# Optimization experiments

Hardware: AMD Instinct MI355X
Metric: run time of the kernel (lower is better)

## Reference

```python
import jax, jax.numpy as jnp
import numpy as np

H = 16
D_MODEL = 1024
D_K = D_MODEL // H
WINDOW = 50
ROPE_BASE = 10000.0


def _rope_tables(seq_len, dim, dtype):
    inv_freq = 1.0 / (ROPE_BASE ** (jnp.arange(0, dim, 2, dtype=jnp.float32) / dim))
    t = jnp.arange(seq_len, dtype=jnp.float32)
    freqs = t[:, None] * inv_freq[None, :]          # [S, dim/2]
    emb = jnp.concatenate([freqs, freqs], axis=-1)  # [S, dim]
    return jnp.cos(emb).astype(dtype), jnp.sin(emb).astype(dtype)


def _rotate_half(x):
    d = x.shape[-1] // 2
    return jnp.concatenate([-x[..., d:], x[..., :d]], axis=-1)


def setup_inputs() -> dict:
    key = jax.random.key(0)
    ks = jax.random.split(key, 11)
    B, S = 2, 2048
    scale = 1.0 / np.sqrt(D_MODEL)
    inp = {
        'query': jax.random.normal(ks[0], (B, S, D_MODEL), jnp.float32),
        'key':   jax.random.normal(ks[1], (B, S, D_MODEL), jnp.float32),
        'value': jax.random.normal(ks[2], (B, S, D_MODEL), jnp.float32),
        'Wq': jax.random.normal(ks[3], (D_MODEL, D_MODEL), jnp.float32) * scale,
        'bq': jnp.zeros((D_MODEL,), jnp.float32),
        'Wk': jax.random.normal(ks[4], (D_MODEL, D_MODEL), jnp.float32) * scale,
        'bk': jnp.zeros((D_MODEL,), jnp.float32),
        'Wv': jax.random.normal(ks[5], (D_MODEL, D_MODEL), jnp.float32) * scale,
        'bv': jnp.zeros((D_MODEL,), jnp.float32),
        'Wo': jax.random.normal(ks[6], (D_MODEL, D_MODEL), jnp.float32) * scale,
        'bo': jnp.zeros((D_MODEL,), jnp.float32),
    }
    return inp


def reference(query, key, value, Wq, bq, Wk, bk, Wv, bv, Wo, bo):
    B, S, _ = query.shape
    # QKV projections (torch Linear: x @ W.T + b), split into heads -> [B,H,S,Dk]
    def proj(x, W, b):
        return (x @ W.T + b).reshape(B, S, H, D_K).transpose(0, 2, 1, 3)
    q = proj(query, Wq, bq)
    k = proj(key, Wk, bk)
    v = proj(value, Wv, bv)

    cos, sin = _rope_tables(S, D_K, q.dtype)  # [S, Dk]
    q = q * cos + _rotate_half(q) * sin
    k = k * cos + _rotate_half(k) * sin

    scores = jnp.einsum('bhqd,bhkd->bhqk', q, k) / np.sqrt(D_K)
    # sliding-window mask: |i-j| <= WINDOW
    idx = jnp.arange(S)
    dist = jnp.abs(idx[None, :] - idx[:, None])  # [S, S]
    scores = jnp.where(dist <= WINDOW, scores, jnp.asarray(-1e9, scores.dtype))

    p = jax.nn.softmax(scores, axis=-1)
    out = jnp.einsum('bhqk,bhkd->bhqd', p, v)          # [B,H,S,Dk]
    out = out.transpose(0, 2, 1, 3).reshape(B, S, D_MODEL)
    return out @ Wo.T + bo
```

## Files before the change

kernel.cpp:

```cpp
#include <hip/hip_runtime.h>
#include <hip/hip_bf16.h>
#include <math.h>

typedef __bf16 bf16_t;
typedef __bf16 bf16x8 __attribute__((ext_vector_type(8)));
typedef float floatx4 __attribute__((ext_vector_type(4)));
typedef unsigned int u32;

#define NHEAD 16

__device__ __forceinline__ void gload_lds16(const void* g, void* l) {
    __builtin_amdgcn_global_load_lds((const __attribute__((address_space(1))) u32*)g,
                                     (__attribute__((address_space(3))) u32*)l, 16, 0, 0);
}

__global__ __launch_bounds__(256) void k_prep(
    const float* __restrict__ q, const float* __restrict__ k, const float* __restrict__ v,
    const float* __restrict__ wq, const float* __restrict__ wk,
    const float* __restrict__ wv, const float* __restrict__ wo,
    bf16_t* __restrict__ Xq, bf16_t* __restrict__ Xk, bf16_t* __restrict__ Xv,
    bf16_t* __restrict__ Wqb, bf16_t* __restrict__ Wkb, bf16_t* __restrict__ Wvb,
    bf16_t* __restrict__ Wob, float* __restrict__ ct, float* __restrict__ st)
{
    int b = blockIdx.x;
    if (b < 8192) {
        const float* src; bf16_t* dst; int off;
        if      (b < 2048) { src = q;  dst = Xq;  off = b; }
        else if (b < 4096) { src = k;  dst = Xk;  off = b - 2048; }
        else if (b < 6144) { src = v;  dst = Xv;  off = b - 4096; }
        else if (b < 6656) { src = wq; dst = Wqb; off = b - 6144; }
        else if (b < 7168) { src = wk; dst = Wkb; off = b - 6656; }
        else if (b < 7680) { src = wv; dst = Wvb; off = b - 7168; }
        else               { src = wo; dst = Wob; off = b - 7680; }
        int i = (off * 256 + threadIdx.x) * 8;
        float4 a = *(const float4*)(src + i);
        float4 c = *(const float4*)(src + i + 4);
        bf16x8 o;
        o[0]=(bf16_t)a.x; o[1]=(bf16_t)a.y; o[2]=(bf16_t)a.z; o[3]=(bf16_t)a.w;
        o[4]=(bf16_t)c.x; o[5]=(bf16_t)c.y; o[6]=(bf16_t)c.z; o[7]=(bf16_t)c.w;
        *(bf16x8*)(dst + i) = o;
    } else {
        int idx = (b - 8192) * 256 + threadIdx.x;
        int s = idx >> 5, i = idx & 31;
        float e = (float)(2 * i) / 64.0f;
        float invf = 1.0f / powf(10000.0f, e);
        float ang = (float)s * invf;
        ct[idx] = cosf(ang);
        st[idx] = sinf(ang);
    }
}


__global__ __launch_bounds__(256,3) void k_gemm_qkv(
    const bf16_t* __restrict__ Xq, const bf16_t* __restrict__ Xk, const bf16_t* __restrict__ Xv,
    const bf16_t* __restrict__ Wqb, const bf16_t* __restrict__ Wkb, const bf16_t* __restrict__ Wvb,
    const float* __restrict__ bq, const float* __restrict__ bk, const float* __restrict__ bv,
    bf16_t* __restrict__ Qr, bf16_t* __restrict__ Kr, bf16_t* __restrict__ Vh,
    const float* __restrict__ ct, const float* __restrict__ st)
{
    __shared__ __align__(16) bf16_t As[2][4096];
    __shared__ __align__(16) bf16_t Bs[2][4096];

    int b0 = blockIdx.x;
    int wg = (b0 & 7) * 96 + (b0 >> 3);
    int id  = wg >> 8;
    int bid = wg & 255;

    const bf16_t* A   = (id==0) ? Xq  : (id==1) ? Xk  : Xv;
    const bf16_t* Wt  = (id==0) ? Wqb : (id==1) ? Wkb : Wvb;
    const float*  bias= (id==0) ? bq  : (id==1) ? bk  : bv;
    bf16_t* out = (id==0) ? Qr : (id==1) ? Kr : Vh;
    bool do_rope = (id < 2);

    int bm = (bid >> 3) << 7;
    int bn = (bid & 7) << 7;
    int tid = threadIdx.x;
    int l = tid & 63, wid = tid >> 6;
    int wr = wid >> 1, wc = wid & 1;
    int fr = l & 15, kg = l >> 4;

    floatx4 acc[4][4];
    #pragma unroll
    for (int i = 0; i < 4; ++i)
        #pragma unroll
        for (int j = 0; j < 4; ++j) acc[i][j] = (floatx4){0.f,0.f,0.f,0.f};

    int srow = tid >> 2;
    int scol = ((tid & 3) ^ (srow & 3)) << 3;
    const bf16_t* Ap0 = A  + ((size_t)(bm + srow) << 10) + scol;
    const bf16_t* Ap1 = A  + ((size_t)(bm + 64 + srow) << 10) + scol;
    const bf16_t* Bp0 = Wt + ((size_t)(bn + srow) << 10) + scol;
    const bf16_t* Bp1 = Wt + ((size_t)(bn + 64 + srow) << 10) + scol;

    gload_lds16(Ap0, &As[0][tid << 3]);
    gload_lds16(Ap1, &As[0][(tid + 256) << 3]);
    gload_lds16(Bp0, &Bs[0][tid << 3]);
    gload_lds16(Bp1, &Bs[0][(tid + 256) << 3]);
    __syncthreads();

    int a_off = fr * 64 + ((kg ^ (fr & 3)) << 4);
    int cur = 0;
    for (int t = 0; t < 32; ++t) {
        if (t < 31) {
            int k0 = (t + 1) << 5;
            gload_lds16(Ap0 + k0, &As[cur ^ 1][tid << 3]);
            gload_lds16(Ap1 + k0, &As[cur ^ 1][(tid + 256) << 3]);
            gload_lds16(Bp0 + k0, &Bs[cur ^ 1][tid << 3]);
            gload_lds16(Bp1 + k0, &Bs[cur ^ 1][(tid + 256) << 3]);
        }
        bf16x8 af[4], bfr[4];
        #pragma unroll
        for (int i = 0; i < 4; ++i)
            af[i]  = *(const bf16x8*)((const char*)As[cur] + (((wr << 2) + i) << 10) + a_off);
        #pragma unroll
        for (int j = 0; j < 4; ++j)
            bfr[j] = *(const bf16x8*)((const char*)Bs[cur] + (((wc << 2) + j) << 10) + a_off);
        #pragma unroll
        for (int i = 0; i < 4; ++i)
            #pragma unroll
            for (int j = 0; j < 4; ++j)
                acc[i][j] = __builtin_amdgcn_mfma_f32_16x16x32_bf16(af[i], bfr[j], acc[i][j], 0, 0, 0);
        __syncthreads();
        cur ^= 1;
    }

    int h = (bn + (wc<<6)) >> 6;
    #pragma unroll
    for (int i = 0; i < 4; ++i) {
        #pragma unroll
        for (int r = 0; r < 4; ++r) {
            int m  = bm + (wr<<6) + (i<<4) + (kg<<2) + r;
            int b_ = m >> 11, s_ = m & 2047;
            size_t ob = ((((size_t)(b_*NHEAD + h)) << 11) + s_) << 6;
            if (do_rope) {
                #pragma unroll
                for (int j = 0; j < 2; ++j) {
                    int d = (j<<4) + fr;
                    float lo = acc[i][j][r]   + bias[bn + (wc<<6) + d];
                    float hv = acc[i][j+2][r] + bias[bn + (wc<<6) + d + 32];
                    float c = ct[(s_<<5) + d], sn = st[(s_<<5) + d];
                    out[ob + d]      = (bf16_t)(lo*c - hv*sn);
                    out[ob + d + 32] = (bf16_t)(hv*c + lo*sn);
                }
            } else {
                #pragma unroll
                for (int j = 0; j < 4; ++j) {
                    int d = (j<<4) + fr;
                    out[ob + d] = (bf16_t)(acc[i][j][r] + bias[bn + (wc<<6) + d]);
                }
            }
        }
    }
}

__global__ __launch_bounds__(256,4) void k_gemm_o(
    const bf16_t* __restrict__ A, const bf16_t* __restrict__ Wt,
    const float* __restrict__ bias, float* __restrict__ out)
{
    __shared__ __align__(16) bf16_t As[2][2048];
    __shared__ __align__(16) bf16_t Bs[2][2048];

    int b0 = blockIdx.x;
    int wg = (b0 & 7) * 128 + (b0 >> 3);
    int bm = (wg >> 4) << 6;
    int bn = (wg & 15) << 6;
    int tid = threadIdx.x;
    int l = tid & 63, wid = tid >> 6;
    int fr = l & 15, kg = l >> 4;

    floatx4 acc[4];
    #pragma unroll
    for (int j = 0; j < 4; ++j) acc[j] = (floatx4){0.f,0.f,0.f,0.f};

    int srow = tid >> 2;
    int scol = ((tid & 3) ^ (srow & 3)) << 3;
    const bf16_t* Ap = A  + ((size_t)(bm + srow) << 10) + scol;
    const bf16_t* Bp = Wt + ((size_t)(bn + srow) << 10) + scol;

    gload_lds16(Ap, &As[0][tid << 3]);
    gload_lds16(Bp, &Bs[0][tid << 3]);
    __syncthreads();

    int a_off = fr * 64 + ((kg ^ (fr & 3)) << 4);
    int cur = 0;
    for (int t = 0; t < 32; ++t) {
        if (t < 31) {
            int k0 = (t + 1) << 5;
            gload_lds16(Ap + k0, &As[cur ^ 1][tid << 3]);
            gload_lds16(Bp + k0, &Bs[cur ^ 1][tid << 3]);
        }
        bf16x8 af, bfr[4];
        af = *(const bf16x8*)((const char*)As[cur] + (wid << 10) + a_off);
        #pragma unroll
        for (int j = 0; j < 4; ++j)
            bfr[j] = *(const bf16x8*)((const char*)Bs[cur] + (j << 10) + a_off);
        #pragma unroll
        for (int j = 0; j < 4; ++j)
            acc[j] = __builtin_amdgcn_mfma_f32_16x16x32_bf16(af, bfr[j], acc[j], 0, 0, 0);
        __syncthreads();
        cur ^= 1;
    }

    #pragma unroll
    for (int r = 0; r < 4; ++r) {
        int m = bm + (wid << 4) + (kg << 2) + r;
        #pragma unroll
        for (int j = 0; j < 4; ++j) {
            int n = bn + (j << 4) + fr;
            out[((size_t)m << 10) + n] = acc[j][r] + bias[n];
        }
    }
}

__global__ __launch_bounds__(256,3) void k_attn(
    const bf16_t* __restrict__ Qr, const bf16_t* __restrict__ Kr,
    const bf16_t* __restrict__ Vh, bf16_t* __restrict__ AO)
{
    __shared__ char smem[51200];
    char* KsPs = smem;
    char* VtB  = smem + 25600;

    int q0 = blockIdx.x << 6;
    int h = blockIdx.y, b_ = blockIdx.z;
    int kstart = q0 - 64; if (kstart < 0) kstart = 0;
    int kend   = q0 + 128; if (kend > 2048) kend = 2048;
    int NR = kend - kstart;

    int tid = threadIdx.x, l = tid & 63, w = tid >> 6;
    int lane16 = l & 15, hi8 = (l >> 4) << 3;

    const bf16_t* Kbase = Kr + (((((size_t)(b_*NHEAD + h)) << 11) + kstart) << 6);
    const bf16_t* Vbase = Vh + (((((size_t)(b_*NHEAD + h)) << 11) + kstart) << 6);

    #pragma unroll
    for (int it = 0; it < 6; ++it) {
        int c = tid + (it << 8);
        int y = c << 4;
        int row = y >> 7, oz = y & 127;
        int srw = row < NR ? row : NR - 1;
        int src = (srw << 7) + (oz ^ ((row & 7) << 4));
        gload_lds16((const char*)Kbase + src, KsPs + y);
    }
    #pragma unroll
    for (int it = 0; it < 6; ++it) {
        int c = tid + (it << 8);
        int jd = c >> 3, d0 = (c & 7) << 3;
        int js = jd < NR ? jd : NR - 1;
        bf16x8 v8 = *(const bf16x8*)(Vbase + (js << 6) + d0);
        #pragma unroll
        for (int t = 0; t < 8; ++t) {
            int d = d0 + t;
            int byte = d * 400 + (((jd << 1)) ^ (((d >> 3) & 7) << 4));
            *(bf16_t*)(VtB + byte) = v8[t];
        }
    }
    int qs = q0 + (w << 4) + lane16;
    const bf16_t* Qbase = Qr + (((((size_t)(b_*NHEAD + h)) << 11) + qs) << 6);
    bf16x8 qf0 = *(const bf16x8*)(Qbase + hi8);
    bf16x8 qf1 = *(const bf16x8*)(Qbase + 32 + hi8);

    __syncthreads();

    floatx4 sc[12];
    #pragma unroll
    for (int kt = 0; kt < 12; ++kt) {
        int row = (kt << 4) + lane16;
        int base = (row << 7) + (hi8 << 1);
        int swz = (row & 7) << 4;
        bf16x8 kf0 = *(const bf16x8*)(KsPs + (base ^ swz));
        bf16x8 kf1 = *(const bf16x8*)(KsPs + ((base + 64) ^ swz));
        floatx4 a = (floatx4){0.f,0.f,0.f,0.f};
        a = __builtin_amdgcn_mfma_f32_16x16x32_bf16(qf0, kf0, a, 0, 0, 0);
        a = __builtin_amdgcn_mfma_f32_16x16x32_bf16(qf1, kf1, a, 0, 0, 0);
        sc[kt] = a;
    }

    float inv_[4];
    #pragma unroll
    for (int r = 0; r < 4; ++r) {
        int qrow = q0 + (w << 4) + ((l >> 4) << 2) + r;
        float mx = -1e30f;
        #pragma unroll
        for (int kt = 0; kt < 12; ++kt) {
            int ks = kstart + (kt << 4) + lane16;
            int dd = qrow - ks; dd = dd < 0 ? -dd : dd;
            float sv = sc[kt][r] * 0.125f;
            sv = (dd <= 50 && ks < kend) ? sv : -1e30f;
            sc[kt][r] = sv;
            mx = fmaxf(mx, sv);
        }
        #pragma unroll
        for (int off = 1; off < 16; off <<= 1) mx = fmaxf(mx, __shfl_xor(mx, off));
        float sum = 0.f;
        #pragma unroll
        for (int kt = 0; kt < 12; ++kt) {
            float p = __expf(sc[kt][r] - mx);
            sc[kt][r] = p;
            sum += p;
        }
        #pragma unroll
        for (int off = 1; off < 16; off <<= 1) sum += __shfl_xor(sum, off);
        inv_[r] = 1.0f / sum;
    }

    __syncthreads();

    char* PwB = KsPs + w * 6400;
    #pragma unroll
    for (int r = 0; r < 4; ++r) {
        int prow = ((l >> 4) << 2) + r;
        int pm = ((prow >> 2) & 3) << 4;
        #pragma unroll
        for (int kt = 0; kt < 12; ++kt) {
            int keyoff = ((kt << 4) + lane16) << 1;
            *(bf16_t*)(PwB + prow * 400 + (keyoff ^ pm)) = (bf16_t)(sc[kt][r] * inv_[r]);
        }
    }

    floatx4 oc[4];
    #pragma unroll
    for (int dt = 0; dt < 4; ++dt) oc[dt] = (floatx4){0.f,0.f,0.f,0.f};
    int pm_r = ((lane16 >> 2) & 3) << 4;
    #pragma unroll
    for (int ks = 0; ks < 6; ++ks) {
        int keyoff = ((ks << 5) + hi8) << 1;
        bf16x8 pf = *(const bf16x8*)(PwB + lane16 * 400 + (keyoff ^ pm_r));
        #pragma unroll
        for (int dt = 0; dt < 4; ++dt) {
            int d = (dt << 4) + lane16;
            bf16x8 vf = *(const bf16x8*)(VtB + d * 400 + (keyoff ^ (((d >> 3) & 7) << 4)));
            oc[dt] = __builtin_amdgcn_mfma_f32_16x16x32_bf16(pf, vf, oc[dt], 0, 0, 0);
        }
    }
    #pragma unroll
    for (int dt = 0; dt < 4; ++dt)
        #pragma unroll
        for (int r = 0; r < 4; ++r) {
            int qq = q0 + (w << 4) + ((l >> 4) << 2) + r;
            AO[(((size_t)(b_ * 2048 + qq)) << 10) + (h << 6) + (dt << 4) + lane16] = (bf16_t)oc[dt][r];
        }
}

extern "C" void kernel_launch(void* const* d_in, const int* in_sizes, int n_in,
                              void* d_out, int out_size, void* d_ws, size_t ws_size,
                              hipStream_t stream)
{
    const float* query = (const float*)d_in[0];
    const float* key_  = (const float*)d_in[1];
    const float* value = (const float*)d_in[2];
    const float* Wq = (const float*)d_in[3];
    const float* bq = (const float*)d_in[4];
    const float* Wk = (const float*)d_in[5];
    const float* bk = (const float*)d_in[6];
    const float* Wv = (const float*)d_in[7];
    const float* bv = (const float*)d_in[8];
    const float* Wo = (const float*)d_in[9];
    const float* bo = (const float*)d_in[10];

    char* ws = (char*)d_ws;
    bf16_t* Xq  = (bf16_t*)(ws);
    bf16_t* Xk  = (bf16_t*)(ws + 8388608);
    bf16_t* Xv  = (bf16_t*)(ws + 16777216);
    bf16_t* Wqb = (bf16_t*)(ws + 25165824);
    bf16_t* Wkb = (bf16_t*)(ws + 27262976);
    bf16_t* Wvb = (bf16_t*)(ws + 29360128);
    bf16_t* Wob = (bf16_t*)(ws + 31457280);
    bf16_t* Qr  = (bf16_t*)(ws + 33554432);
    bf16_t* Kr  = (bf16_t*)(ws + 41943040);
    bf16_t* Vh  = (bf16_t*)(ws + 50331648);
    bf16_t* AO  = (bf16_t*)(ws + 58720256);
    float*  ct  = (float*)(ws + 67108864);
    float*  st  = (float*)(ws + 67371008);

    k_prep<<<8448, 256, 0, stream>>>(query, key_, value, Wq, Wk, Wv, Wo,
                                     Xq, Xk, Xv, Wqb, Wkb, Wvb, Wob, ct, st);
    k_gemm_qkv<<<768, 256, 0, stream>>>(Xq, Xk, Xv, Wqb, Wkb, Wvb,
                                        bq, bk, bv, Qr, Kr, Vh, ct, st);
    k_attn<<<dim3(32, 16, 2), 256, 0, stream>>>(Qr, Kr, Vh, AO);
    k_gemm_o<<<1024, 256, 0, stream>>>(AO, Wob, bo, (float*)d_out);
}
```

Baseline: 94.11 us.

## Fuse fp32-to-bf16 activation conversion into QKV GEMM loads

The QKV GEMM now stages the fp32 activations directly into LDS with an XOR swizzle and converts them to bf16 while building MFMA fragments. The separate prep pass that wrote bf16 copies of query/key/value is removed. This cuts a full read and write of the activations through global memory, at the cost of doubling LDS use for the A tile and adding conversion work inside the GEMM loop. Separately, the V-transpose staging in attention now packs two rows into one 32-bit LDS store instead of issuing scalar 16-bit stores.

```diff
diff --git a/kernel.cpp b/kernel.cpp
--- a/kernel.cpp
+++ b/kernel.cpp
@@ -6,6 +6,7 @@
 typedef __bf16 bf16x8 __attribute__((ext_vector_type(8)));
 typedef float floatx4 __attribute__((ext_vector_type(4)));
 typedef unsigned int u32;
+typedef unsigned short u16;
 
 #define NHEAD 16
 
@@ -14,33 +15,32 @@
                                      (__attribute__((address_space(3))) u32*)l, 16, 0, 0);
 }
 
+__device__ __forceinline__ bf16x8 cvt8(float4 a, float4 b) {
+    bf16x8 o;
+    o[0]=(bf16_t)a.x; o[1]=(bf16_t)a.y; o[2]=(bf16_t)a.z; o[3]=(bf16_t)a.w;
+    o[4]=(bf16_t)b.x; o[5]=(bf16_t)b.y; o[6]=(bf16_t)b.z; o[7]=(bf16_t)b.w;
+    return o;
+}
+
 __global__ __launch_bounds__(256) void k_prep(
-    const float* __restrict__ q, const float* __restrict__ k, const float* __restrict__ v,
     const float* __restrict__ wq, const float* __restrict__ wk,
     const float* __restrict__ wv, const float* __restrict__ wo,
-    bf16_t* __restrict__ Xq, bf16_t* __restrict__ Xk, bf16_t* __restrict__ Xv,
     bf16_t* __restrict__ Wqb, bf16_t* __restrict__ Wkb, bf16_t* __restrict__ Wvb,
     bf16_t* __restrict__ Wob, float* __restrict__ ct, float* __restrict__ st)
 {
     int b = blockIdx.x;
-    if (b < 8192) {
+    if (b < 2048) {
         const float* src; bf16_t* dst; int off;
-        if      (b < 2048) { src = q;  dst = Xq;  off = b; }
-        else if (b < 4096) { src = k;  dst = Xk;  off = b - 2048; }
-        else if (b < 6144) { src = v;  dst = Xv;  off = b - 4096; }
-        else if (b < 6656) { src = wq; dst = Wqb; off = b - 6144; }
-        else if (b < 7168) { src = wk; dst = Wkb; off = b - 6656; }
-        else if (b < 7680) { src = wv; dst = Wvb; off = b - 7168; }
-        else               { src = wo; dst = Wob; off = b - 7680; }
+        if      (b < 512)  { src = wq; dst = Wqb; off = b; }
+        else if (b < 1024) { src = wk; dst = Wkb; off = b - 512; }
+        else if (b < 1536) { src = wv; dst = Wvb; off = b - 1024; }
+        else               { src = wo; dst = Wob; off = b - 1536; }
         int i = (off * 256 + threadIdx.x) * 8;
         float4 a = *(const float4*)(src + i);
         float4 c = *(const float4*)(src + i + 4);
-        bf16x8 o;
-        o[0]=(bf16_t)a.x; o[1]=(bf16_t)a.y; o[2]=(bf16_t)a.z; o[3]=(bf16_t)a.w;
-        o[4]=(bf16_t)c.x; o[5]=(bf16_t)c.y; o[6]=(bf16_t)c.z; o[7]=(bf16_t)c.w;
-        *(bf16x8*)(dst + i) = o;
+        *(bf16x8*)(dst + i) = cvt8(a, c);
     } else {
-        int idx = (b - 8192) * 256 + threadIdx.x;
+        int idx = (b - 2048) * 256 + threadIdx.x;
         int s = idx >> 5, i = idx & 31;
         float e = (float)(2 * i) / 64.0f;
         float invf = 1.0f / powf(10000.0f, e);
@@ -50,15 +50,14 @@
     }
 }
 
-
 __global__ __launch_bounds__(256,3) void k_gemm_qkv(
-    const bf16_t* __restrict__ Xq, const bf16_t* __restrict__ Xk, const bf16_t* __restrict__ Xv,
+    const float* __restrict__ Xq, const float* __restrict__ Xk, const float* __restrict__ Xv,
     const bf16_t* __restrict__ Wqb, const bf16_t* __restrict__ Wkb, const bf16_t* __restrict__ Wvb,
     const float* __restrict__ bq, const float* __restrict__ bk, const float* __restrict__ bv,
     bf16_t* __restrict__ Qr, bf16_t* __restrict__ Kr, bf16_t* __restrict__ Vh,
     const float* __restrict__ ct, const float* __restrict__ st)
 {
-    __shared__ __align__(16) bf16_t As[2][4096];
+    __shared__ __align__(16) float  As[2][4096];
     __shared__ __align__(16) bf16_t Bs[2][4096];
 
     int b0 = blockIdx.x;
@@ -66,7 +65,7 @@
     int id  = wg >> 8;
     int bid = wg & 255;
 
-    const bf16_t* A   = (id==0) ? Xq  : (id==1) ? Xk  : Xv;
+    const float*  A   = (id==0) ? Xq  : (id==1) ? Xk  : Xv;
     const bf16_t* Wt  = (id==0) ? Wqb : (id==1) ? Wkb : Wvb;
     const float*  bias= (id==0) ? bq  : (id==1) ? bk  : bv;
     bf16_t* out = (id==0) ? Qr : (id==1) ? Kr : Vh;
@@ -85,36 +84,49 @@
         #pragma unroll
         for (int j = 0; j < 4; ++j) acc[i][j] = (floatx4){0.f,0.f,0.f,0.f};
 
-    int srow = tid >> 2;
-    int scol = ((tid & 3) ^ (srow & 3)) << 3;
-    const bf16_t* Ap0 = A  + ((size_t)(bm + srow) << 10) + scol;
-    const bf16_t* Ap1 = A  + ((size_t)(bm + 64 + srow) << 10) + scol;
-    const bf16_t* Bp0 = Wt + ((size_t)(bn + srow) << 10) + scol;
-    const bf16_t* Bp1 = Wt + ((size_t)(bn + 64 + srow) << 10) + scol;
-
-    gload_lds16(Ap0, &As[0][tid << 3]);
-    gload_lds16(Ap1, &As[0][(tid + 256) << 3]);
+    const char* ApB[4];
+    #pragma unroll
+    for (int it = 0; it < 4; ++it) {
+        int c = tid + (it << 8);
+        int row = c >> 3;
+        int zp = ((c & 7) << 4) ^ ((row & 7) << 4);
+        ApB[it] = (const char*)A + ((size_t)(bm + row) << 12) + zp;
+    }
+    int srowB = tid >> 2, scolB = (tid & 3) << 3;
+    const bf16_t* Bp0 = Wt + ((size_t)(bn + srowB) << 10) + scolB;
+    const bf16_t* Bp1 = Wt + ((size_t)(bn + 64 + srowB) << 10) + scolB;
+
+    #pragma unroll
+    for (int it = 0; it < 4; ++it)
+        gload_lds16(ApB[it], (char*)As[0] + ((tid + (it << 8)) << 4));
     gload_lds16(Bp0, &Bs[0][tid << 3]);
     gload_lds16(Bp1, &Bs[0][(tid + 256) << 3]);
     __syncthreads();
 
-    int a_off = fr * 64 + ((kg ^ (fr & 3)) << 4);
+    int swA = (fr & 7) << 4;
     int cur = 0;
     for (int t = 0; t < 32; ++t) {
         if (t < 31) {
-            int k0 = (t + 1) << 5;
-            gload_lds16(Ap0 + k0, &As[cur ^ 1][tid << 3]);
-            gload_lds16(Ap1 + k0, &As[cur ^ 1][(tid + 256) << 3]);
-            gload_lds16(Bp0 + k0, &Bs[cur ^ 1][tid << 3]);
-            gload_lds16(Bp1 + k0, &Bs[cur ^ 1][(tid + 256) << 3]);
-        }
+            int kA = (t + 1) << 7;
+            int kB = (t + 1) << 5;
+            #pragma unroll
+            for (int it = 0; it < 4; ++it)
+                gload_lds16(ApB[it] + kA, (char*)As[cur ^ 1] + ((tid + (it << 8)) << 4));
+            gload_lds16(Bp0 + kB, &Bs[cur ^ 1][tid << 3]);
+            gload_lds16(Bp1 + kB, &Bs[cur ^ 1][(tid + 256) << 3]);
+        }
+        const char* Ac = (const char*)As[cur];
         bf16x8 af[4], bfr[4];
         #pragma unroll
-        for (int i = 0; i < 4; ++i)
-            af[i]  = *(const bf16x8*)((const char*)As[cur] + (((wr << 2) + i) << 10) + a_off);
+        for (int i = 0; i < 4; ++i) {
+            int rowbyte = ((wr << 6) + (i << 4) + fr) << 7;
+            float4 lo = *(const float4*)(Ac + rowbyte + ((kg << 5) ^ swA));
+            float4 hi = *(const float4*)(Ac + rowbyte + (((kg << 5) + 16) ^ swA));
+            af[i] = cvt8(lo, hi);
+        }
         #pragma unroll
         for (int j = 0; j < 4; ++j)
-            bfr[j] = *(const bf16x8*)((const char*)Bs[cur] + (((wc << 2) + j) << 10) + a_off);
+            bfr[j] = *(const bf16x8*)&Bs[cur][((wc << 6) + (j << 4) + fr) * 32 + (kg << 3)];
         #pragma unroll
         for (int i = 0; i < 4; ++i)
             #pragma unroll
@@ -244,14 +256,20 @@
     #pragma unroll
     for (int it = 0; it < 6; ++it) {
         int c = tid + (it << 8);
-        int jd = c >> 3, d0 = (c & 7) << 3;
-        int js = jd < NR ? jd : NR - 1;
-        bf16x8 v8 = *(const bf16x8*)(Vbase + (js << 6) + d0);
-        #pragma unroll
-        for (int t = 0; t < 8; ++t) {
-            int d = d0 + t;
-            int byte = d * 400 + (((jd << 1)) ^ (((d >> 3) & 7) << 4));
-            *(bf16_t*)(VtB + byte) = v8[t];
+        int jd2 = c >> 4;
+        int dq  = (c & 15) << 2;
+        int j0 = jd2 << 1, j1 = j0 + 1;
+        int j0c = j0 < NR ? j0 : NR - 1;
+        int j1c = j1 < NR ? j1 : NR - 1;
+        ushort4 v0 = *(const ushort4*)(Vbase + (j0c << 6) + dq);
+        ushort4 v1 = *(const ushort4*)(Vbase + (j1c << 6) + dq);
+        u16 a0[4] = {(u16)v0.x,(u16)v0.y,(u16)v0.z,(u16)v0.w};
+        u16 a1[4] = {(u16)v1.x,(u16)v1.y,(u16)v1.z,(u16)v1.w};
+        #pragma unroll
+        for (int t = 0; t < 4; ++t) {
+            int d = dq + t;
+            u32 pair = (u32)a0[t] | ((u32)a1[t] << 16);
+            *(u32*)(VtB + d * 400 + ((jd2 << 2) ^ (((d >> 3) & 7) << 4))) = pair;
         }
     }
     int qs = q0 + (w << 4) + lane16;
@@ -358,23 +376,19 @@
     const float* bo = (const float*)d_in[10];
 
     char* ws = (char*)d_ws;
-    bf16_t* Xq  = (bf16_t*)(ws);
-    bf16_t* Xk  = (bf16_t*)(ws + 8388608);
-    bf16_t* Xv  = (bf16_t*)(ws + 16777216);
-    bf16_t* Wqb = (bf16_t*)(ws + 25165824);
-    bf16_t* Wkb = (bf16_t*)(ws + 27262976);
-    bf16_t* Wvb = (bf16_t*)(ws + 29360128);
-    bf16_t* Wob = (bf16_t*)(ws + 31457280);
-    bf16_t* Qr  = (bf16_t*)(ws + 33554432);
-    bf16_t* Kr  = (bf16_t*)(ws + 41943040);
-    bf16_t* Vh  = (bf16_t*)(ws + 50331648);
-    bf16_t* AO  = (bf16_t*)(ws + 58720256);
-    float*  ct  = (float*)(ws + 67108864);
-    float*  st  = (float*)(ws + 67371008);
-
-    k_prep<<<8448, 256, 0, stream>>>(query, key_, value, Wq, Wk, Wv, Wo,
-                                     Xq, Xk, Xv, Wqb, Wkb, Wvb, Wob, ct, st);
-    k_gemm_qkv<<<768, 256, 0, stream>>>(Xq, Xk, Xv, Wqb, Wkb, Wvb,
+    bf16_t* Wqb = (bf16_t*)(ws);
+    bf16_t* Wkb = (bf16_t*)(ws + 2097152);
+    bf16_t* Wvb = (bf16_t*)(ws + 4194304);
+    bf16_t* Wob = (bf16_t*)(ws + 6291456);
+    bf16_t* Qr  = (bf16_t*)(ws + 8388608);
+    bf16_t* Kr  = (bf16_t*)(ws + 16777216);
+    bf16_t* Vh  = (bf16_t*)(ws + 25165824);
+    bf16_t* AO  = (bf16_t*)(ws + 33554432);
+    float*  ct  = (float*)(ws + 41943040);
+    float*  st  = (float*)(ws + 42205184);
+
+    k_prep<<<2304, 256, 0, stream>>>(Wq, Wk, Wv, Wo, Wqb, Wkb, Wvb, Wob, ct, st);
+    k_gemm_qkv<<<768, 256, 0, stream>>>(query, key_, value, Wqb, Wkb, Wvb,
                                         bq, bk, bv, Qr, Kr, Vh, ct, st);
     k_attn<<<dim3(32, 16, 2), 256, 0, stream>>>(Qr, Kr, Vh, AO);
     k_gemm_o<<<1024, 256, 0, stream>>>(AO, Wob, bo, (float*)d_out);
```

After: 92.17 us, median of 2. 1.02x faster.
